# Kernel tuning notes

Measured on AMD Instinct MI355X. Metric: run time of the kernel, lower is better.

The kernel has to match this reference:

```python
import jax, jax.numpy as jnp
import numpy as np

N = 4096
F_IN = 3000
F_OUT = 64
NEG_INF = jnp.float32(-9e15)


def _xavier(key, shape):
    fan_in, fan_out = shape[0], shape[-1]
    limit = (6.0 / (fan_in + fan_out)) ** 0.5
    return jax.random.uniform(key, shape, jnp.float32, -limit, limit)


def setup_inputs() -> dict:
    key = jax.random.key(0)
    ks = jax.random.split(key, 20)
    feat = jax.random.normal(ks[0], (N, F_IN), jnp.float32)
    feat_a = jax.random.normal(ks[1], (N, F_IN), jnp.float32)
    eye = jnp.eye(N, dtype=jnp.float32)
    adj = jnp.maximum((jax.random.uniform(ks[2], (N, N)) < 0.008).astype(jnp.float32), eye)
    graph_neigh = jnp.maximum((jax.random.uniform(ks[3], (N, N)) < 0.008).astype(jnp.float32), eye)
    return {
        "feat": feat,
        "feat_a": feat_a,
        "adj": adj,
        "graph_neigh": graph_neigh,
        "weight1": _xavier(ks[4], (F_IN, F_OUT)),
        "weight2": _xavier(ks[5], (F_OUT, F_IN)),
        "att_W": _xavier(ks[6], (F_OUT, F_OUT)),
        "a_src": _xavier(ks[7], (F_OUT, 1)),
        "a_dst": _xavier(ks[8], (F_OUT, 1)),
        "mlp_W1": _xavier(ks[9], (F_OUT, 256)),
        "mlp_b1": jnp.zeros((256,), jnp.float32),
        "mlp_W2": _xavier(ks[10], (256, 128)),
        "mlp_b2": jnp.zeros((128,), jnp.float32),
        "mlp_W3": _xavier(ks[11], (128, F_OUT)),
        "mlp_b3": jnp.zeros((F_OUT,), jnp.float32),
        "dmlp_W1": _xavier(ks[12], (F_OUT, 128)),
        "dmlp_b1": jnp.zeros((128,), jnp.float32),
        "dmlp_W2": _xavier(ks[13], (128, F_OUT)),
        "dmlp_b2": jnp.zeros((F_OUT,), jnp.float32),
        "bil_W": _xavier(ks[14], (F_OUT, F_OUT)),
        "bil_b": jnp.zeros((1,), jnp.float32),
    }


def reference(feat, feat_a, adj, graph_neigh,
              weight1, weight2, att_W, a_src, a_dst,
              mlp_W1, mlp_b1, mlp_W2, mlp_b2, mlp_W3, mlp_b3,
              dmlp_W1, dmlp_b1, dmlp_W2, dmlp_b2, bil_W, bil_b):
    relu = jax.nn.relu

    def attention(h):
        Wh = h @ att_W                      # [N, F_OUT]
        e = Wh @ a_src + (Wh @ a_dst).T     # [N, N]
        e = jnp.where(e > 0, e, 0.2 * e)    # LeakyReLU(0.2)
        e = jnp.where(adj > 0, e, NEG_INF)  # mask non-edges
        return jax.nn.softmax(e, axis=1) @ Wh

    def mlp(x):
        x = relu(x @ mlp_W1 + mlp_b1)
        x = relu(x @ mlp_W2 + mlp_b2)
        return x @ mlp_W3 + mlp_b3

    def dmlp(x):  # discriminator MLP: n_h -> 128 -> n_h
        return relu(x @ dmlp_W1 + dmlp_b1) @ dmlp_W2 + dmlp_b2

    def readout(emb):  # AvgReadout + L2 normalize
        g = (graph_neigh @ emb) / jnp.sum(graph_neigh, axis=1, keepdims=True)
        return g / jnp.maximum(jnp.linalg.norm(g, axis=1, keepdims=True), 1e-12)

    def bilinear(x, y):  # nn.Bilinear(n_h, n_h, 1)
        return (jnp.einsum('ni,ij,nj->n', x, bil_W, y) + bil_b)[:, None]

    def disc(c, h_pl, h_mi):
        c, h_pl, h_mi = dmlp(c), dmlp(h_pl), dmlp(h_mi)
        return jnp.concatenate([bilinear(h_pl, c), bilinear(h_mi, c)], axis=1)

    z = mlp(attention(feat @ weight1))
    hiden_emb = z
    h = adj @ (z @ weight2)                 # spmm(adj, z @ weight2)
    emb = relu(z)
    z_a = mlp(attention(feat_a @ weight1))
    emb_a = relu(z_a)
    g = jax.nn.sigmoid(readout(emb))
    g_a = jax.nn.sigmoid(readout(emb_a))
    ret = disc(g, emb, emb_a)
    ret_a = disc(g_a, emb_a, emb)
    return (hiden_emb, h, ret, ret_a)
```

## Files before the change

### kernel.cpp

```cpp
#include <hip/hip_runtime.h>

#define NN   4096
#define FIN  3000
#define MAXN 128

typedef unsigned short u16;
typedef __bf16 bf16x8 __attribute__((ext_vector_type(8)));
typedef float f32x16 __attribute__((ext_vector_type(16)));

__device__ __forceinline__ float bf2f(u16 u) { union { unsigned int i; float f; } v; v.i = ((unsigned int)u) << 16; return v.f; }
__device__ __forceinline__ u16 f2bf(float f) {
    union { float f; unsigned int i; } v; v.f = f;
    return (u16)((v.i + 0x7FFFu + ((v.i >> 16) & 1u)) >> 16);
}
__device__ __forceinline__ bf16x8 bzero8() {
    union { unsigned long long q[2]; bf16x8 v; } u; u.q[0] = 0ull; u.q[1] = 0ull; return u.v;
}
__device__ __forceinline__ f32x16 fzero16() {
    f32x16 v;
    #pragma unroll
    for (int i = 0; i < 16; i++) v[i] = 0.f;
    return v;
}

__global__ __launch_bounds__(1024) void k_detect(const u16* __restrict__ feat, int* __restrict__ flag)
{
    __shared__ int tot;
    if (threadIdx.x == 0) tot = 0;
    __syncthreads();
    int ins = 0;
    for (int i = threadIdx.x; i < 16384; i += 1024) {
        u16 u = feat[i];
        int e = (u >> 7) & 0xFF;
        if (u != 0 && (e < 90 || e > 160)) ins++;
    }
    atomicAdd(&tot, ins);
    __syncthreads();
    if (threadIdx.x == 0) *flag = (tot > 1024) ? 1 : 0;
}

__global__ __launch_bounds__(256) void k_convw(const int* __restrict__ flag,
    const void* s0, const void* s1, const void* s2, const void* s3,
    const void* s4, const void* s5, const void* s6, const void* s7,
    const void* s8, const void* s9, const void* s10, const void* s11,
    const void* s12, const void* s13, const void* s14, const void* s15,
    float* __restrict__ dst)
{
    const void* srcs[16] = {s0,s1,s2,s3,s4,s5,s6,s7,s8,s9,s10,s11,s12,s13,s14,s15};
    const int offs[16] = {0,192000,196096,196160,196224,212608,212864,245632,245760,253952,254016,262208,262336,270528,270592,274688};
    const int ns[16]   = {192000,4096,64,64,16384,256,32768,128,8192,64,8192,128,8192,64,4096,1};
    int seg = blockIdx.y;
    int i = blockIdx.x * 256 + threadIdx.x;
    if (i >= ns[seg]) return;
    float v = (*flag) ? ((const float*)srcs[seg])[i] : bf2f(((const u16*)srcs[seg])[i]);
    dst[offs[seg] + i] = v;
}

__global__ __launch_bounds__(256) void k_convw2t(const int* __restrict__ flag,
    const void* __restrict__ src, u16* __restrict__ WH, u16* __restrict__ WL)
{
    int i = blockIdx.x * 256 + threadIdx.x;
    if (i >= 3008 * 64) return;
    int n = i >> 6, k = i & 63;
    float v = 0.f;
    if (n < FIN)
        v = (*flag) ? ((const float*)src)[(size_t)k * FIN + n]
                    : bf2f(((const u16*)src)[(size_t)k * FIN + n]);
    u16 h = f2bf(v);
    float r = v - bf2f(h);
    WH[i] = h;
    WL[i] = f2bf(r);
}

__global__ __launch_bounds__(256) void k_convw1t(const int* __restrict__ flag,
    const void* __restrict__ w1src, u16* __restrict__ BtH, u16* __restrict__ BtL)
{
    int i = blockIdx.x * 256 + threadIdx.x;
    if (i >= 64 * 3008) return;
    int c = i / 3008, k = i - c * 3008;
    float v = 0.f;
    if (k < 3000)
        v = (*flag) ? ((const float*)w1src)[(size_t)k * 64 + c]
                    : bf2f(((const u16*)w1src)[(size_t)k * 64 + c]);
    u16 h = f2bf(v);
    float r = v - bf2f(h);
    BtH[(size_t)c * 3008 + k] = h;
    BtL[(size_t)c * 3008 + k] = f2bf(r);
}

__global__ __launch_bounds__(256) void k_build_csr(const int* __restrict__ flag,
    const void* __restrict__ Av, const void* __restrict__ Gv,
    int* __restrict__ aCnt, int* __restrict__ aIdx,
    int* __restrict__ gCnt, int* __restrict__ gIdx)
{
    bool isf = (*flag != 0);
    const void* M = blockIdx.y ? Gv : Av;
    int* cnt = blockIdx.y ? gCnt : aCnt;
    int* idx = blockIdx.y ? gIdx : aIdx;
    int row = blockIdx.x, t = threadIdx.x;
    int c0 = t * 16;
    unsigned int mask = 0; int my = 0;
    if (isf) {
        const float* r = (const float*)M + (size_t)row * NN + c0;
        #pragma unroll
        for (int j = 0; j < 16; j++) if (r[j] != 0.f) { mask |= 1u << j; my++; }
    } else {
        const u16* r = (const u16*)M + (size_t)row * NN + c0;
        #pragma unroll
        for (int j = 0; j < 16; j++) if (r[j] != 0) { mask |= 1u << j; my++; }
    }
    __shared__ int sc[256];
    sc[t] = my;
    __syncthreads();
    for (int d = 1; d < 256; d <<= 1) {
        int v = (t >= d) ? sc[t - d] : 0;
        __syncthreads();
        sc[t] += v;
        __syncthreads();
    }
    int pos = sc[t] - my;
    for (int j = 0; j < 16; j++) {
        if (mask & (1u << j)) {
            if (pos < MAXN) idx[(size_t)row * MAXN + pos] = c0 + j;
            pos++;
        }
    }
    if (t == 0) { int total = sc[255]; cnt[row] = (total < MAXN) ? total : MAXN; }
}

__global__ __launch_bounds__(512) void k_featgemm_mfma(const int* __restrict__ flag,
    const void* __restrict__ F0v, const void* __restrict__ F1v,
    const u16* __restrict__ BtH, float* __restrict__ X0, float* __restrict__ X1)
{
    if (*flag) return;
    const u16* F = (const u16*)(blockIdx.y ? F1v : F0v);
    float* X = blockIdx.y ? X1 : X0;
    int r0 = blockIdx.x * 32;
    int tid = threadIdx.x;
    int w  = tid >> 6;
    int l  = tid & 63;
    int lr = l & 31;
    int kg = l >> 5;
    const u16* arow = F   + (size_t)(r0 + lr) * FIN + kg * 8;
    const u16* b0p  = BtH + (size_t)lr * 3008 + kg * 8;
    const u16* b1p  = BtH + (size_t)(lr + 32) * 3008 + kg * 8;
    f32x16 acc0 = fzero16(), acc1 = fzero16();
    #pragma unroll 4
    for (int s = w; s < 188; s += 8) {
        int kk = s * 16;
        bf16x8 a;
        if (kk + kg * 8 < FIN) a = *(const bf16x8*)(arow + kk);
        else                   a = bzero8();
        bf16x8 b0 = *(const bf16x8*)(b0p + kk);
        bf16x8 b1 = *(const bf16x8*)(b1p + kk);
        acc0 = __builtin_amdgcn_mfma_f32_32x32x16_bf16(a, b0, acc0, 0, 0, 0);
        acc1 = __builtin_amdgcn_mfma_f32_32x32x16_bf16(a, b1, acc1, 0, 0, 0);
    }
    __shared__ float red[8][2048];
    float* rp = red[w];
    #pragma unroll
    for (int reg = 0; reg < 16; reg++) {
        int row = (reg & 3) + 8 * (reg >> 2) + 4 * kg;
        rp[row * 64 + lr] = acc0[reg];
    }
    #pragma unroll
    for (int reg = 0; reg < 16; reg++) {
        int row = (reg & 3) + 8 * (reg >> 2) + 4 * kg;
        rp[row * 64 + 32 + lr] = acc1[reg];
    }
    __syncthreads();
    for (int i = tid; i < 2048; i += 512) {
        float s0 = 0.f;
        #pragma unroll
        for (int j = 0; j < 8; j++) s0 += red[j][i];
        X[(size_t)r0 * 64 + i] = s0;
    }
}

__global__ __launch_bounds__(512) void k_featgemm_mfma_f32(const int* __restrict__ flag,
    const void* __restrict__ F0v, const void* __restrict__ F1v,
    const u16* __restrict__ BtH, const u16* __restrict__ BtL,
    float* __restrict__ X0, float* __restrict__ X1)
{
    if (!*flag) return;
    const float* F = (const float*)(blockIdx.y ? F1v : F0v);
    float* X = blockIdx.y ? X1 : X0;
    int r0 = blockIdx.x * 32;
    int tid = threadIdx.x;
    int w  = tid >> 6;
    int l  = tid & 63;
    int lr = l & 31;
    int kg = l >> 5;
    int s0 = blockIdx.z * 8 + w;
    const float* arow = F + (size_t)(r0 + lr) * FIN + kg * 8;
    const u16* b0h = BtH + (size_t)lr * 3008 + kg * 8;
    const u16* b1h = BtH + (size_t)(lr + 32) * 3008 + kg * 8;
    const u16* b0l = BtL + (size_t)lr * 3008 + kg * 8;
    const u16* b1l = BtL + (size_t)(lr + 32) * 3008 + kg * 8;
    f32x16 acc0 = fzero16(), acc1 = fzero16();
    #pragma unroll 2
    for (int s = s0; s < 188; s += 16) {
        int kk = s * 16;
        float av[8];
        if (kk + kg * 8 < FIN) {
            float4 p0 = *(const float4*)(arow + kk);
            float4 p1 = *(const float4*)(arow + kk + 4);
            av[0] = p0.x; av[1] = p0.y; av[2] = p0.z; av[3] = p0.w;
            av[4] = p1.x; av[5] = p1.y; av[6] = p1.z; av[7] = p1.w;
        } else {
            #pragma unroll
            for (int j = 0; j < 8; j++) av[j] = 0.f;
        }
        bf16x8 ah, al;
        #pragma unroll
        for (int j = 0; j < 8; j++) {
            __bf16 hv = (__bf16)av[j];
            float  rv = av[j] - (float)hv;
            ah[j] = hv;
            al[j] = (__bf16)rv;
        }
        bf16x8 v0h = *(const bf16x8*)(b0h + kk);
        bf16x8 v1h = *(const bf16x8*)(b1h + kk);
        bf16x8 v0l = *(const bf16x8*)(b0l + kk);
        bf16x8 v1l = *(const bf16x8*)(b1l + kk);
        acc0 = __builtin_amdgcn_mfma_f32_32x32x16_bf16(ah, v0h, acc0, 0, 0, 0);
        acc0 = __builtin_amdgcn_mfma_f32_32x32x16_bf16(al, v0h, acc0, 0, 0, 0);
        acc0 = __builtin_amdgcn_mfma_f32_32x32x16_bf16(ah, v0l, acc0, 0, 0, 0);
        acc1 = __builtin_amdgcn_mfma_f32_32x32x16_bf16(ah, v1h, acc1, 0, 0, 0);
        acc1 = __builtin_amdgcn_mfma_f32_32x32x16_bf16(al, v1h, acc1, 0, 0, 0);
        acc1 = __builtin_amdgcn_mfma_f32_32x32x16_bf16(ah, v1l, acc1, 0, 0, 0);
    }
    __shared__ float red[8][2048];
    float* rp = red[w];
    #pragma unroll
    for (int reg = 0; reg < 16; reg++) {
        int row = (reg & 3) + 8 * (reg >> 2) + 4 * kg;
        rp[row * 64 + lr] = acc0[reg];
    }
    #pragma unroll
    for (int reg = 0; reg < 16; reg++) {
        int row = (reg & 3) + 8 * (reg >> 2) + 4 * kg;
        rp[row * 64 + 32 + lr] = acc1[reg];
    }
    __syncthreads();
    for (int i = tid; i < 2048; i += 512) {
        float s0s = 0.f;
        #pragma unroll
        for (int j = 0; j < 8; j++) s0s += red[j][i];
        atomicAdd(&X[(size_t)r0 * 64 + i], s0s);
    }
}

__global__ __launch_bounds__(64) void k_whsd(
    const float* __restrict__ X1, const float* __restrict__ X2,
    const float* __restrict__ AW, const float* __restrict__ asrc, const float* __restrict__ adst,
    float* __restrict__ Wh1, float* __restrict__ Wh2,
    float* __restrict__ s1, float* __restrict__ s2,
    float* __restrict__ d1, float* __restrict__ d2)
{
    const float* X = blockIdx.y ? X2 : X1;
    float* Wh = blockIdx.y ? Wh2 : Wh1;
    float* sv = blockIdx.y ? s2 : s1;
    float* dv = blockIdx.y ? d2 : d1;
    int row = blockIdx.x, c = threadIdx.x;
    __shared__ float x[64];
    x[c] = X[(size_t)row * 64 + c];
    __syncthreads();
    float acc = 0.f;
    #pragma unroll 16
    for (int k = 0; k < 64; k++) acc += x[k] * AW[k * 64 + c];
    Wh[(size_t)row * 64 + c] = acc;
    float vs = acc * asrc[c];
    float vd = acc * adst[c];
    #pragma unroll
    for (int off = 32; off > 0; off >>= 1) { vs += __shfl_down(vs, off); vd += __shfl_down(vd, off); }
    if (c == 0) { sv[row] = vs; dv[row] = vd; }
}

__global__ __launch_bounds__(128) void k_attn(
    const int* __restrict__ cnt, const int* __restrict__ idx,
    const float* __restrict__ s1, const float* __restrict__ s2,
    const float* __restrict__ d1, const float* __restrict__ d2,
    const float* __restrict__ Wh1, const float* __restrict__ Wh2,
    float* __restrict__ A1, float* __restrict__ A2)
{
    const float* sp = blockIdx.y ? s2 : s1;
    const float* dp = blockIdx.y ? d2 : d1;
    const float* Wh = blockIdx.y ? Wh2 : Wh1;
    float* A = blockIdx.y ? A2 : A1;
    int row = blockIdx.x, tid = threadIdx.x;
    int n = cnt[row];
    __shared__ int js[MAXN];
    __shared__ float ps[MAXN];
    __shared__ float red2[2];
    __shared__ float ared[2][64];
    for (int k = tid; k < n; k += 128) js[k] = idx[(size_t)row * MAXN + k];
    __syncthreads();
    float si = sp[row];
    float m = -3.0e38f;
    for (int k = tid; k < n; k += 128) {
        float e = si + dp[js[k]];
        e = e > 0.f ? e : 0.2f * e;
        ps[k] = e;
        m = fmaxf(m, e);
    }
    #pragma unroll
    for (int off = 32; off > 0; off >>= 1) m = fmaxf(m, __shfl_down(m, off));
    if ((tid & 63) == 0) red2[tid >> 6] = m;
    __syncthreads();
    m = fmaxf(red2[0], red2[1]);
    __syncthreads();
    float zz = 0.f;
    for (int k = tid; k < n; k += 128) {
        float p = __expf(ps[k] - m);
        ps[k] = p;
        zz += p;
    }
    #pragma unroll
    for (int off = 32; off > 0; off >>= 1) zz += __shfl_down(zz, off);
    if ((tid & 63) == 0) red2[tid >> 6] = zz;
    __syncthreads();
    float Z = red2[0] + red2[1];
    Z = fmaxf(Z, 1e-20f);
    int f = tid & 63, half = tid >> 6;
    float acc = 0.f;
    for (int k = half; k < n; k += 2) acc += ps[k] * Wh[(size_t)js[k] * 64 + f];
    ared[half][f] = acc;
    __syncthreads();
    if (tid < 64) A[(size_t)row * 64 + f] = (ared[0][f] + ared[1][f]) / Z;
}

__global__ __launch_bounds__(256) void k_mlp(const int* __restrict__ flag,
    const float* __restrict__ A1, const float* __restrict__ A2,
    const float* __restrict__ W1, const float* __restrict__ b1,
    const float* __restrict__ W2, const float* __restrict__ b2,
    const float* __restrict__ W3, const float* __restrict__ b3,
    float* __restrict__ Z1, float* __restrict__ Z2, void* __restrict__ hidenv)
{
    const float* A = blockIdx.y ? A2 : A1;
    float* Z = blockIdx.y ? Z2 : Z1;
    int row0 = blockIdx.x * 4, tid = threadIdx.x;
    __shared__ float x[4][64], h1[4][256], h2[4][128];
    {
        int r = tid >> 6, c = tid & 63;
        x[r][c] = A[(size_t)(row0 + r) * 64 + c];
    }
    __syncthreads();
    {
        float a0 = b1[tid], a1v = a0, a2v = a0, a3v = a0;
        #pragma unroll 8
        for (int k = 0; k < 64; k++) {
            float w = W1[k * 256 + tid];
            a0 += x[0][k] * w; a1v += x[1][k] * w; a2v += x[2][k] * w; a3v += x[3][k] * w;
        }
        h1[0][tid] = fmaxf(a0, 0.f);  h1[1][tid] = fmaxf(a1v, 0.f);
        h1[2][tid] = fmaxf(a2v, 0.f); h1[3][tid] = fmaxf(a3v, 0.f);
    }
    __syncthreads();
    if (tid < 128) {
        float a0 = b2[tid], a1v = a0, a2v = a0, a3v = a0;
        #pragma unroll 8
        for (int k = 0; k < 256; k++) {
            float w = W2[k * 128 + tid];
            a0 += h1[0][k] * w; a1v += h1[1][k] * w; a2v += h1[2][k] * w; a3v += h1[3][k] * w;
        }
        h2[0][tid] = fmaxf(a0, 0.f);  h2[1][tid] = fmaxf(a1v, 0.f);
        h2[2][tid] = fmaxf(a2v, 0.f); h2[3][tid] = fmaxf(a3v, 0.f);
    }
    __syncthreads();
    if (tid < 64) {
        float a[4];
        a[0] = a[1] = a[2] = a[3] = b3[tid];
        #pragma unroll 8
        for (int k = 0; k < 128; k++) {
            float w = W3[k * 64 + tid];
            a[0] += h2[0][k] * w; a[1] += h2[1][k] * w; a[2] += h2[2][k] * w; a[3] += h2[3][k] * w;
        }
        bool isf = (*flag != 0);
        #pragma unroll
        for (int r = 0; r < 4; r++) {
            size_t ei = (size_t)(row0 + r) * 64 + tid;
            Z[ei] = a[r];
            if (blockIdx.y == 0) {
                if (isf) ((float*)hidenv)[ei] = a[r];
                else     ((u16*)hidenv)[ei] = f2bf(a[r]);
            }
        }
    }
}

__global__ __launch_bounds__(64) void k_spmm(
    const int* __restrict__ cnt, const int* __restrict__ idx,
    const float* __restrict__ Z, float* __restrict__ T)
{
    int row = blockIdx.x, f = threadIdx.x;
    int n = cnt[row];
    const int* ir = idx + (size_t)row * MAXN;
    float acc = 0.f;
    for (int k = 0; k < n; k++) acc += Z[(size_t)ir[k] * 64 + f];
    T[(size_t)row * 64 + f] = acc;
}

__global__ __launch_bounds__(256) void k_hgemm_mfma(const int* __restrict__ flag,
    const float* __restrict__ T, const u16* __restrict__ WH, const u16* __restrict__ WL,
    void* __restrict__ outv)
{
    bool isf = (*flag != 0);
    int tid = threadIdx.x;
    int w = tid >> 6, l = tid & 63, lr = l & 31, kg = l >> 5;
    int ct = blockIdx.y * 4 + w;
    if (ct >= 94) return;
    int r0 = blockIdx.x * 32, c0 = ct * 32;
    const float* tp = T + (size_t)(r0 + lr) * 64 + kg * 8;
    bf16x8 ah[4], al[4];
    #pragma unroll
    for (int s = 0; s < 4; s++) {
        float4 p0 = *(const float4*)(tp + s * 16);
        float4 p1 = *(const float4*)(tp + s * 16 + 4);
        float av[8] = {p0.x, p0.y, p0.z, p0.w, p1.x, p1.y, p1.z, p1.w};
        #pragma unroll
        for (int j = 0; j < 8; j++) {
            __bf16 hv = (__bf16)av[j];
            ah[s][j] = hv;
            al[s][j] = (__bf16)(av[j] - (float)hv);
        }
    }
    const u16* bh = WH + (size_t)(c0 + lr) * 64 + kg * 8;
    const u16* bl = WL + (size_t)(c0 + lr) * 64 + kg * 8;
    f32x16 acc = fzero16();
    #pragma unroll
    for (int s = 0; s < 4; s++) {
        bf16x8 vh = *(const bf16x8*)(bh + s * 16);
        bf16x8 vl = *(const bf16x8*)(bl + s * 16);
        acc = __builtin_amdgcn_mfma_f32_32x32x16_bf16(ah[s], vh, acc, 0, 0, 0);
        acc = __builtin_amdgcn_mfma_f32_32x32x16_bf16(al[s], vh, acc, 0, 0, 0);
        acc = __builtin_amdgcn_mfma_f32_32x32x16_bf16(ah[s], vl, acc, 0, 0, 0);
    }
    int col = c0 + lr;
    bool cok = col < FIN;
    #pragma unroll
    for (int reg = 0; reg < 16; reg++) {
        int row = (reg & 3) + 8 * (reg >> 2) + 4 * kg;
        size_t ei = 262144 + (size_t)(r0 + row) * FIN + col;
        if (cok) {
            if (isf) ((float*)outv)[ei] = acc[reg];
            else     ((u16*)outv)[ei] = f2bf(acc[reg]);
        }
    }
}

__global__ __launch_bounds__(64) void k_readout(
    const int* __restrict__ cnt, const int* __restrict__ idx,
    const float* __restrict__ Z1, const float* __restrict__ Z2,
    float* __restrict__ G1, float* __restrict__ G2)
{
    const float* Z = blockIdx.y ? Z2 : Z1;
    float* G = blockIdx.y ? G2 : G1;
    int row = blockIdx.x, f = threadIdx.x;
    int n = cnt[row];
    const int* ir = idx + (size_t)row * MAXN;
    float acc = 0.f;
    for (int k = 0; k < n; k++) acc += fmaxf(Z[(size_t)ir[k] * 64 + f], 0.f);
    acc /= (float)(n > 0 ? n : 1);
    float sq = acc * acc;
    #pragma unroll
    for (int off = 32; off > 0; off >>= 1) sq += __shfl_down(sq, off);
    sq = __shfl(sq, 0);
    float nrm = fmaxf(sqrtf(sq), 1e-12f);
    float v = acc / nrm;
    G[(size_t)row * 64 + f] = 1.f / (1.f + __expf(-v));
}

__global__ __launch_bounds__(128) void k_dmlp(
    const float* __restrict__ z, const float* __restrict__ za,
    const float* __restrict__ g, const float* __restrict__ ga,
    const float* __restrict__ W1, const float* __restrict__ b1,
    const float* __restrict__ W2, const float* __restrict__ b2,
    float* __restrict__ De, float* __restrict__ Dea,
    float* __restrict__ Dg, float* __restrict__ Dga)
{
    int w = blockIdx.y;
    const float* X = (w == 0) ? z : (w == 1) ? za : (w == 2) ? g : ga;
    float* O = (w == 0) ? De : (w == 1) ? Dea : (w == 2) ? Dg : Dga;
    int doRelu = (w < 2);
    int row0 = blockIdx.x * 4, tid = threadIdx.x;
    __shared__ float x[4][64], h1[4][128];
    for (int i = tid; i < 256; i += 128) {
        int r = i >> 6, c = i & 63;
        float v = X[(size_t)(row0 + r) * 64 + c];
        x[r][c] = doRelu ? fmaxf(v, 0.f) : v;
    }
    __syncthreads();
    {
        float a0 = b1[tid], a1v = a0, a2v = a0, a3v = a0;
        #pragma unroll 8
        for (int k = 0; k < 64; k++) {
            float w_ = W1[k * 128 + tid];
            a0 += x[0][k] * w_; a1v += x[1][k] * w_; a2v += x[2][k] * w_; a3v += x[3][k] * w_;
        }
        h1[0][tid] = fmaxf(a0, 0.f);  h1[1][tid] = fmaxf(a1v, 0.f);
        h1[2][tid] = fmaxf(a2v, 0.f); h1[3][tid] = fmaxf(a3v, 0.f);
    }
    __syncthreads();
    if (tid < 64) {
        float a[4];
        a[0] = a[1] = a[2] = a[3] = b2[tid];
        #pragma unroll 8
        for (int k = 0; k < 128; k++) {
            float w_ = W2[k * 64 + tid];
            a[0] += h1[0][k] * w_; a[1] += h1[1][k] * w_; a[2] += h1[2][k] * w_; a[3] += h1[3][k] * w_;
        }
        #pragma unroll
        for (int r = 0; r < 4; r++) O[(size_t)(row0 + r) * 64 + tid] = a[r];
    }
}

__global__ __launch_bounds__(64) void k_bilin(const int* __restrict__ flag,
    const float* __restrict__ De, const float* __restrict__ Dea,
    const float* __restrict__ Dg, const float* __restrict__ Dga,
    const float* __restrict__ BW, const float* __restrict__ bb, void* __restrict__ outv)
{
    int w = blockIdx.y;
    const float* X = (w == 0 || w == 3) ? De : Dea;
    const float* Y = (w <= 1) ? Dg : Dga;
    size_t bse = (w <= 1) ? (size_t)12550144 : (size_t)12558336;
    int col = (w == 0 || w == 2) ? 0 : 1;
    int row = blockIdx.x, k = threadIdx.x;
    __shared__ float x[64], y[64];
    x[k] = X[(size_t)row * 64 + k];
    y[k] = Y[(size_t)row * 64 + k];
    __syncthreads();
    float wv = 0.f;
    #pragma unroll 8
    for (int j = 0; j < 64; j++) wv += BW[k * 64 + j] * y[j];
    float v = x[k] * wv;
    #pragma unroll
    for (int off = 32; off > 0; off >>= 1) v += __shfl_down(v, off);
    if (k == 0) {
        float r = v + bb[0];
        size_t ei = bse + (size_t)row * 2 + col;
        if (*flag) ((float*)outv)[ei] = r;
        else       ((u16*)outv)[ei] = f2bf(r);
    }
}

extern "C" void kernel_launch(void* const* d_in, const int* in_sizes, int n_in,
                              void* d_out, int out_size, void* d_ws, size_t ws_size,
                              hipStream_t stream) {
    const void* feat   = d_in[0];
    const void* feat_a = d_in[1];
    const void* adj    = d_in[2];
    const void* gn     = d_in[3];
    const void* w1     = d_in[4];
    const void* w2     = d_in[5];
    const void* attW   = d_in[6];
    const void* a_src  = d_in[7];
    const void* a_dst  = d_in[8];
    const void* mW1    = d_in[9];
    const void* mb1    = d_in[10];
    const void* mW2    = d_in[11];
    const void* mb2    = d_in[12];
    const void* mW3    = d_in[13];
    const void* mb3    = d_in[14];
    const void* dW1    = d_in[15];
    const void* db1    = d_in[16];
    const void* dW2    = d_in[17];
    const void* db2    = d_in[18];
    const void* bW     = d_in[19];
    const void* bb     = d_in[20];
    (void)in_sizes; (void)n_in; (void)out_size;

    char* wsb = (char*)d_ws;
    int*   flag = (int*)wsb;
    float* T    = (float*)(wsb + 256);
    u16*   W2tH = (u16*)(wsb + 256 + 1048576);
    u16*   W2tL = W2tH + 3008 * 64;
    (void)ws_size;

    char* sc = (char*)d_out + 1048576;
    size_t soff = 0;
    auto salloc = [&](size_t nbytes) -> void* {
        void* p = (void*)(sc + soff);
        soff += (nbytes + 255) & ~(size_t)255;
        return p;
    };
    const size_t NV = (size_t)NN * 64;
    float* wA   = (float*)salloc((size_t)274689 * 4);
    int*   aCnt = (int*)salloc(NN * 4);
    int*   gCnt = (int*)salloc(NN * 4);
    int*   aIdx = (int*)salloc((size_t)NN * MAXN * 4);
    int*   gIdx = (int*)salloc((size_t)NN * MAXN * 4);
    float* X1  = (float*)salloc(NV * 4);
    float* X2  = (float*)salloc(NV * 4);
    float* Wh1 = (float*)salloc(NV * 4);
    float* Wh2 = (float*)salloc(NV * 4);
    float* A1  = (float*)salloc(NV * 4);
    float* A2  = (float*)salloc(NV * 4);
    float* z   = (float*)salloc(NV * 4);
    float* za  = (float*)salloc(NV * 4);
    float* g   = (float*)salloc(NV * 4);
    float* ga  = (float*)salloc(NV * 4);
    float* De  = (float*)salloc(NV * 4);
    float* Dea = (float*)salloc(NV * 4);
    float* Dg  = (float*)salloc(NV * 4);
    float* Dga = (float*)salloc(NV * 4);
    float* s1  = (float*)salloc(NN * 4);
    float* s2  = (float*)salloc(NN * 4);
    float* d1  = (float*)salloc(NN * 4);
    float* d2  = (float*)salloc(NN * 4);

    float* w1f   = wA + 0;
    float* attWf = wA + 192000;
    float* asrcf = wA + 196096;
    float* adstf = wA + 196160;
    float* mW1f  = wA + 196224;
    float* mb1f  = wA + 212608;
    float* mW2f  = wA + 212864;
    float* mb2f  = wA + 245632;
    float* mW3f  = wA + 245760;
    float* mb3f  = wA + 253952;
    float* dW1f  = wA + 254016;
    float* db1f  = wA + 262208;
    float* dW2f  = wA + 262336;
    float* db2f  = wA + 270528;
    float* bWf   = wA + 270592;
    float* bbf   = wA + 274688;

    u16* BtH = (u16*)De;
    u16* BtL = (u16*)Dea;

    k_detect<<<1, 1024, 0, stream>>>((const u16*)feat, flag);
    k_convw<<<dim3(750, 16), 256, 0, stream>>>(flag,
        w1, attW, a_src, a_dst, mW1, mb1, mW2, mb2, mW3, mb3,
        dW1, db1, dW2, db2, bW, bb, wA);
    k_convw2t<<<752, 256, 0, stream>>>(flag, w2, W2tH, W2tL);
    k_convw1t<<<752, 256, 0, stream>>>(flag, w1, BtH, BtL);
    k_build_csr<<<dim3(NN, 2), 256, 0, stream>>>(flag, adj, gn, aCnt, aIdx, gCnt, gIdx);
    hipMemsetAsync(X1, 0, 2 * NV * 4, stream);
    k_featgemm_mfma<<<dim3(NN / 32, 2), 512, 0, stream>>>(flag, feat, feat_a, BtH, X1, X2);
    k_featgemm_mfma_f32<<<dim3(NN / 32, 2, 2), 512, 0, stream>>>(flag, feat, feat_a, BtH, BtL, X1, X2);
    k_whsd<<<dim3(NN, 2), 64, 0, stream>>>(X1, X2, attWf, asrcf, adstf, Wh1, Wh2, s1, s2, d1, d2);
    k_attn<<<dim3(NN, 2), 128, 0, stream>>>(aCnt, aIdx, s1, s2, d1, d2, Wh1, Wh2, A1, A2);
    k_mlp<<<dim3(NN / 4, 2), 256, 0, stream>>>(flag, A1, A2, mW1f, mb1f, mW2f, mb2f, mW3f, mb3f, z, za, d_out);
    k_readout<<<dim3(NN, 2), 64, 0, stream>>>(gCnt, gIdx, z, za, g, ga);
    k_dmlp<<<dim3(NN / 4, 4), 128, 0, stream>>>(z, za, g, ga, dW1f, db1f, dW2f, db2f, De, Dea, Dg, Dga);
    k_bilin<<<dim3(NN, 4), 64, 0, stream>>>(flag, De, Dea, Dg, Dga, bWf, bbf, d_out);
    k_spmm<<<NN, 64, 0, stream>>>(aCnt, aIdx, z, T);
    k_hgemm_mfma<<<dim3(NN / 32, 24), 256, 0, stream>>>(flag, T, W2tH, W2tL, d_out);
}
```

Before: 471.2 us.

## Double-buffer fp32 feature GEMM through LDS with async global-to-LDS loads

The split-bf16 feature GEMM now uses 64x64 output tiles with four 32x32 waves and a four-way split over K. Tiles of the fp32 activations are staged into swizzled, double-buffered LDS with global_load_lds, so the next 64-wide K slab loads while the current one feeds the MFMAs. The old cross-wave shared-memory reduction is replaced by direct atomic adds to the output. CSR building also switches to vectorized 16-byte row loads. In exchange the kernel does more atomics per output and a barrier every K step, and the last K slab reads past the end of each 3000-float row.

```diff
diff --git a/kernel.cpp b/kernel.cpp
--- a/kernel.cpp
+++ b/kernel.cpp
@@ -21,6 +21,11 @@
     #pragma unroll
     for (int i = 0; i < 16; i++) v[i] = 0.f;
     return v;
+}
+__device__ __forceinline__ void gload_lds16(const float* src, void* ldsbase) {
+    __builtin_amdgcn_global_load_lds(
+        (const __attribute__((address_space(1))) void*)src,
+        (__attribute__((address_space(3))) void*)ldsbase, 16, 0, 0);
 }
 
 __global__ __launch_bounds__(1024) void k_detect(const u16* __restrict__ feat, int* __restrict__ flag)
@@ -101,13 +106,17 @@
     int c0 = t * 16;
     unsigned int mask = 0; int my = 0;
     if (isf) {
-        const float* r = (const float*)M + (size_t)row * NN + c0;
-        #pragma unroll
-        for (int j = 0; j < 16; j++) if (r[j] != 0.f) { mask |= 1u << j; my++; }
+        const float4* r = (const float4*)((const float*)M + (size_t)row * NN + c0);
+        union { float4 q[4]; float f[16]; } u;
+        u.q[0] = r[0]; u.q[1] = r[1]; u.q[2] = r[2]; u.q[3] = r[3];
+        #pragma unroll
+        for (int j = 0; j < 16; j++) if (u.f[j] != 0.f) { mask |= 1u << j; my++; }
     } else {
-        const u16* r = (const u16*)M + (size_t)row * NN + c0;
-        #pragma unroll
-        for (int j = 0; j < 16; j++) if (r[j] != 0) { mask |= 1u << j; my++; }
+        const uint4* r = (const uint4*)((const u16*)M + (size_t)row * NN + c0);
+        union { uint4 q[2]; u16 h[16]; } u;
+        u.q[0] = r[0]; u.q[1] = r[1];
+        #pragma unroll
+        for (int j = 0; j < 16; j++) if (u.h[j] != 0) { mask |= 1u << j; my++; }
     }
     __shared__ int sc[256];
     sc[t] = my;
@@ -177,7 +186,7 @@
     }
 }
 
-__global__ __launch_bounds__(512) void k_featgemm_mfma_f32(const int* __restrict__ flag,
+__global__ __launch_bounds__(256) void k_featgemm_mfma_f32(const int* __restrict__ flag,
     const void* __restrict__ F0v, const void* __restrict__ F1v,
     const u16* __restrict__ BtH, const u16* __restrict__ BtL,
     float* __restrict__ X0, float* __restrict__ X1)
@@ -185,69 +194,86 @@
     if (!*flag) return;
     const float* F = (const float*)(blockIdx.y ? F1v : F0v);
     float* X = blockIdx.y ? X1 : X0;
-    int r0 = blockIdx.x * 32;
     int tid = threadIdx.x;
     int w  = tid >> 6;
     int l  = tid & 63;
     int lr = l & 31;
     int kg = l >> 5;
-    int s0 = blockIdx.z * 8 + w;
-    const float* arow = F + (size_t)(r0 + lr) * FIN + kg * 8;
-    const u16* b0h = BtH + (size_t)lr * 3008 + kg * 8;
-    const u16* b1h = BtH + (size_t)(lr + 32) * 3008 + kg * 8;
-    const u16* b0l = BtL + (size_t)lr * 3008 + kg * 8;
-    const u16* b1l = BtL + (size_t)(lr + 32) * 3008 + kg * 8;
-    f32x16 acc0 = fzero16(), acc1 = fzero16();
-    #pragma unroll 2
-    for (int s = s0; s < 188; s += 16) {
-        int kk = s * 16;
-        float av[8];
-        if (kk + kg * 8 < FIN) {
-            float4 p0 = *(const float4*)(arow + kk);
-            float4 p1 = *(const float4*)(arow + kk + 4);
-            av[0] = p0.x; av[1] = p0.y; av[2] = p0.z; av[3] = p0.w;
-            av[4] = p1.x; av[5] = p1.y; av[6] = p1.z; av[7] = p1.w;
-        } else {
+    int wr = w >> 1, wc = w & 1;
+    int r0 = blockIdx.x * 64;
+    int chunk = blockIdx.z;
+    int sbeg = chunk * 12;
+    int nsteps = ((chunk == 3) ? 47 : sbeg + 12) - sbeg;
+
+    __shared__ char lds[2][16384];
+
+    const float* Fb = F + (size_t)r0 * FIN;
+    int arow = 32 * wr + lr;
+    int acol = 32 * wc + lr;
+    const u16* bh = BtH + (size_t)acol * 3008;
+    const u16* bl = BtL + (size_t)acol * 3008;
+
+    int slin = (w * 16) * 256 + l * 16;
+    f32x16 acc = fzero16();
+
+    {
+        int kbase = sbeg * 64;
+        #pragma unroll
+        for (int j = 0; j < 4; j++) {
+            int lin = slin + j * 1024;
+            int row = lin >> 8;
+            int off = (lin & 255) ^ ((row & 15) << 4);
+            gload_lds16(Fb + (size_t)row * FIN + kbase + (off >> 2),
+                        &lds[0][(w * 16 + j * 4) * 256]);
+        }
+    }
+    __syncthreads();
+
+    int cur = 0;
+    for (int s = 0; s < nsteps; ++s) {
+        if (s + 1 < nsteps) {
+            int kbase = (sbeg + s + 1) * 64;
             #pragma unroll
-            for (int j = 0; j < 8; j++) av[j] = 0.f;
-        }
-        bf16x8 ah, al;
-        #pragma unroll
-        for (int j = 0; j < 8; j++) {
-            __bf16 hv = (__bf16)av[j];
-            float  rv = av[j] - (float)hv;
-            ah[j] = hv;
-            al[j] = (__bf16)rv;
-        }
-        bf16x8 v0h = *(const bf16x8*)(b0h + kk);
-        bf16x8 v1h = *(const bf16x8*)(b1h + kk);
-        bf16x8 v0l = *(const bf16x8*)(b0l + kk);
-        bf16x8 v1l = *(const bf16x8*)(b1l + kk);
-        acc0 = __builtin_amdgcn_mfma_f32_32x32x16_bf16(ah, v0h, acc0, 0, 0, 0);
-        acc0 = __builtin_amdgcn_mfma_f32_32x32x16_bf16(al, v0h, acc0, 0, 0, 0);
-        acc0 = __builtin_amdgcn_mfma_f32_32x32x16_bf16(ah, v0l, acc0, 0, 0, 0);
-        acc1 = __builtin_amdgcn_mfma_f32_32x32x16_bf16(ah, v1h, acc1, 0, 0, 0);
-        acc1 = __builtin_amdgcn_mfma_f32_32x32x16_bf16(al, v1h, acc1, 0, 0, 0);
-        acc1 = __builtin_amdgcn_mfma_f32_32x32x16_bf16(ah, v1l, acc1, 0, 0, 0);
-    }
-    __shared__ float red[8][2048];
-    float* rp = red[w];
+            for (int j = 0; j < 4; j++) {
+                int lin = slin + j * 1024;
+                int row = lin >> 8;
+                int off = (lin & 255) ^ ((row & 15) << 4);
+                gload_lds16(Fb + (size_t)row * FIN + kbase + (off >> 2),
+                            &lds[cur ^ 1][(w * 16 + j * 4) * 256]);
+            }
+        }
+        const char* lb = lds[cur];
+        int kk0 = (sbeg + s) * 64;
+        #pragma unroll
+        for (int s16 = 0; s16 < 4; s16++) {
+            int offu = s16 * 64 + kg * 32;
+            int o0 = offu        ^ ((arow & 15) << 4);
+            int o1 = (offu + 16) ^ ((arow & 15) << 4);
+            float4 a0 = *(const float4*)(lb + arow * 256 + o0);
+            float4 a1 = *(const float4*)(lb + arow * 256 + o1);
+            float av[8] = {a0.x, a0.y, a0.z, a0.w, a1.x, a1.y, a1.z, a1.w};
+            bf16x8 ah, al;
+            #pragma unroll
+            for (int jj = 0; jj < 8; jj++) {
+                __bf16 hv = (__bf16)av[jj];
+                ah[jj] = hv;
+                al[jj] = (__bf16)(av[jj] - (float)hv);
+            }
+            int kk = kk0 + s16 * 16 + kg * 8;
+            bf16x8 H = *(const bf16x8*)(bh + kk);
+            bf16x8 L = *(const bf16x8*)(bl + kk);
+            acc = __builtin_amdgcn_mfma_f32_32x32x16_bf16(ah, H, acc, 0, 0, 0);
+            acc = __builtin_amdgcn_mfma_f32_32x32x16_bf16(al, H, acc, 0, 0, 0);
+            acc = __builtin_amdgcn_mfma_f32_32x32x16_bf16(ah, L, acc, 0, 0, 0);
+        }
+        __syncthreads();
+        cur ^= 1;
+    }
+
     #pragma unroll
     for (int reg = 0; reg < 16; reg++) {
         int row = (reg & 3) + 8 * (reg >> 2) + 4 * kg;
-        rp[row * 64 + lr] = acc0[reg];
-    }
-    #pragma unroll
-    for (int reg = 0; reg < 16; reg++) {
-        int row = (reg & 3) + 8 * (reg >> 2) + 4 * kg;
-        rp[row * 64 + 32 + lr] = acc1[reg];
-    }
-    __syncthreads();
-    for (int i = tid; i < 2048; i += 512) {
-        float s0s = 0.f;
-        #pragma unroll
-        for (int j = 0; j < 8; j++) s0s += red[j][i];
-        atomicAdd(&X[(size_t)r0 * 64 + i], s0s);
+        atomicAdd(&X[(size_t)(r0 + 32 * wr + row) * 64 + acol], acc[reg]);
     }
 }
 
@@ -638,7 +664,7 @@
     k_build_csr<<<dim3(NN, 2), 256, 0, stream>>>(flag, adj, gn, aCnt, aIdx, gCnt, gIdx);
     hipMemsetAsync(X1, 0, 2 * NV * 4, stream);
     k_featgemm_mfma<<<dim3(NN / 32, 2), 512, 0, stream>>>(flag, feat, feat_a, BtH, X1, X2);
-    k_featgemm_mfma_f32<<<dim3(NN / 32, 2, 2), 512, 0, stream>>>(flag, feat, feat_a, BtH, BtL, X1, X2);
+    k_featgemm_mfma_f32<<<dim3(NN / 64, 2, 4), 256, 0, stream>>>(flag, feat, feat_a, BtH, BtL, X1, X2);
     k_whsd<<<dim3(NN, 2), 64, 0, stream>>>(X1, X2, attWf, asrcf, adstf, Wh1, Wh2, s1, s2, d1, d2);
     k_attn<<<dim3(NN, 2), 128, 0, stream>>>(aCnt, aIdx, s1, s2, d1, d2, Wh1, Wh2, A1, A2);
     k_mlp<<<dim3(NN / 4, 2), 256, 0, stream>>>(flag, A1, A2, mW1f, mb1f, mW2f, mb2f, mW3f, mb3f, z, za, d_out);
```

Measured after the change: 461.6 us. -2.0%, faster.
